# Optimization experiments

Hardware: AMD Instinct MI355X
Metric: run time of the kernel (lower is better)

The kernel has to match this reference:

```python
import jax, jax.numpy as jnp
import numpy as np

NUM_LONGTERM_MEM = 16  # config.num_longterm_mem


def setup_inputs() -> dict:
    key = jax.random.key(0)
    ks = jax.random.split(key, 9)
    B, T, C, H = 32, 2048, 768, 1536
    s = 0.02
    return {
        "x": jax.random.normal(ks[0], (B, T, C), jnp.float32),
        "Wq": jax.random.normal(ks[1], (C, C), jnp.float32) * s,
        "bq": jax.random.normal(ks[2], (C,), jnp.float32) * s,
        "W0": jax.random.normal(ks[3], (B, H, C), jnp.float32) * s,
        "b0": jax.random.normal(ks[4], (B, H), jnp.float32) * s,
        "W1": jax.random.normal(ks[5], (B, C, H), jnp.float32) * s,
        "b1": jax.random.normal(ks[6], (B, C), jnp.float32) * s,
        "Wo": jax.random.normal(ks[7], (C, C), jnp.float32) * s,
        "bo": jax.random.normal(ks[8], (C,), jnp.float32) * s,
    }


def reference(x, Wq, bq, W0, b0, W1, b1, Wo, bo):
    # x: [B, T, C]. Per-sample memory MLP weights W0 [B,H,C], W1 [B,C,H].
    B, T, C = x.shape
    L = NUM_LONGTERM_MEM
    # query projection (nn.Linear: x @ W^T + b)
    q = jnp.einsum("btc,dc->btd", x, Wq) + bq                       # [B,T,C]
    # per-sample 2-layer memory MLP with SiLU
    h = jax.nn.silu(jnp.einsum("btc,bhc->bth", q, W0) + b0[:, None, :])  # [B,T,H]
    mem = jnp.einsum("bth,bch->btc", h, W1) + b1[:, None, :]        # [B,T,C]
    # adaptive_avg_pool1d over T -> L (T divisible by L => uniform window mean)
    pooled = mem.reshape(B, L, T // L, C).mean(axis=2)              # [B,L,C]
    # output projection
    return jnp.einsum("blc,dc->bld", pooled, Wo) + bo               # [B,L,C]
```

## Files before the change

### kernel.cpp

```cpp
#include <hip/hip_runtime.h>
#include <stdint.h>

#define B_ 32
#define T_ 2048
#define C_ 768
#define H_ 1536
#define L_ 16

typedef unsigned short u16;
typedef __bf16 bf16x8 __attribute__((ext_vector_type(8)));
typedef float f32x4 __attribute__((ext_vector_type(4)));

__device__ __forceinline__ u16 f2bf(float f) {
    union { float f; uint32_t u; } v; v.f = f;
    uint32_t r = (v.u + 0x7fffu + ((v.u >> 16) & 1u)) >> 16;
    return (u16)r;
}

__device__ __forceinline__ float wave_sum(float v) {
    v += __shfl_xor(v, 1);  v += __shfl_xor(v, 2);  v += __shfl_xor(v, 4);
    v += __shfl_xor(v, 8);  v += __shfl_xor(v, 16); v += __shfl_xor(v, 32);
    return v;
}

__global__ void k_cvt(const float* __restrict__ in, u16* __restrict__ out, int n4) {
    int stride = gridDim.x * blockDim.x;
    for (int i = blockIdx.x * blockDim.x + threadIdx.x; i < n4; i += stride) {
        float4 v = reinterpret_cast<const float4*>(in)[i];
        ushort4 o;
        o.x = f2bf(v.x); o.y = f2bf(v.y); o.z = f2bf(v.z); o.w = f2bf(v.w);
        reinterpret_cast<ushort4*>(out)[i] = o;
    }
}

__global__ void k_prep1(const float* __restrict__ Wq, u16* __restrict__ WqTb,
                        const float* __restrict__ W0, u16* __restrict__ W0b,
                        const float* __restrict__ bq, const float* __restrict__ b0,
                        float* __restrict__ b0f, int e0) {
    const int t = threadIdx.x;
    if (blockIdx.x < (unsigned)e0) {
        const int w = t >> 6, lane = t & 63;
        const int nWaves = e0 * 4;
        const float4* bq4 = reinterpret_cast<const float4*>(bq);
        float4 b4_0 = bq4[lane], b4_1 = bq4[64 + lane], b4_2 = bq4[128 + lane];
        for (int rr = blockIdx.x * 4 + w; rr < B_ * H_; rr += nWaves) {
            const float4* src = reinterpret_cast<const float4*>(W0 + (size_t)rr * 768);
            ushort4* dst = reinterpret_cast<ushort4*>(W0b + (size_t)rr * 768);
            float4 v0 = src[lane], v1 = src[64 + lane], v2 = src[128 + lane];
            ushort4 o0, o1, o2;
            o0.x = f2bf(v0.x); o0.y = f2bf(v0.y); o0.z = f2bf(v0.z); o0.w = f2bf(v0.w);
            o1.x = f2bf(v1.x); o1.y = f2bf(v1.y); o1.z = f2bf(v1.z); o1.w = f2bf(v1.w);
            o2.x = f2bf(v2.x); o2.y = f2bf(v2.y); o2.z = f2bf(v2.z); o2.w = f2bf(v2.w);
            dst[lane] = o0; dst[64 + lane] = o1; dst[128 + lane] = o2;
            float dot = v0.x * b4_0.x + v0.y * b4_0.y + v0.z * b4_0.z + v0.w * b4_0.w
                      + v1.x * b4_1.x + v1.y * b4_1.y + v1.z * b4_1.z + v1.w * b4_1.w
                      + v2.x * b4_2.x + v2.y * b4_2.y + v2.z * b4_2.z + v2.w * b4_2.w;
            dot = wave_sum(dot);
            if (lane == 0) b0f[rr] = b0[rr] + dot;
        }
    } else {
        __shared__ u16 tl[64 * 65];
        const int nb = gridDim.x - e0;
        for (int tile = blockIdx.x - e0; tile < 144; tile += nb) {
            int d0 = (tile / 12) * 64, c0 = (tile % 12) * 64;
            __syncthreads();
#pragma unroll
            for (int p = 0; p < 16; ++p) {
                int idx = p * 256 + t;
                int r = idx >> 6, c = idx & 63;
                tl[r * 65 + c] = f2bf(Wq[(size_t)(d0 + r) * 768 + c0 + c]);
            }
            __syncthreads();
#pragma unroll
            for (int p = 0; p < 16; ++p) {
                int idx = p * 256 + t;
                int r = idx >> 6, c = idx & 63;
                WqTb[(size_t)(c0 + r) * 768 + d0 + c] = tl[c * 65 + r];
            }
        }
    }
}

__device__ __forceinline__ void gload16(const u16* g, u16* l) {
    __builtin_amdgcn_global_load_lds((const __attribute__((address_space(1))) void*)g,
                                     (__attribute__((address_space(3))) void*)l, 16, 0, 0);
}

template <int EPI>
__global__ __launch_bounds__(512, 2) void k_gemm9(const u16* __restrict__ Aall,
                                                  const u16* __restrict__ Ball,
                                                  const float* __restrict__ biasall,
                                                  u16* __restrict__ qout,
                                                  float* __restrict__ ph) {
    __shared__ u16 sm[81920];
    const int t = threadIdx.x;
    const int w = t >> 6, lane = t & 63;
    const int wr = w >> 2, wc = w & 3;
    const int l15 = lane & 15, kq = lane >> 4, cx = lane & 7;

    const int gx = gridDim.x, gy = gridDim.y;
    const int nwg = gx * gy * gridDim.z;
    int flat = blockIdx.x + gx * (blockIdx.y + gy * blockIdx.z);
    if ((nwg & 7) == 0) flat = (flat & 7) * (nwg >> 3) + (flat >> 3);
    const int bx = flat % gx;
    const int tmp = flat / gx;
    const int by = tmp % gy;
    const int bz = tmp / gy;

    const int n0 = bx * 256;
    const int m0 = by * 256;
    const u16* A; const u16* Bm; const float* bias;
    if constexpr (EPI == 0) {
        A = Aall + (size_t)m0 * C_;
        Bm = Ball + (size_t)n0 * C_;
        bias = biasall + n0;
    } else {
        A = Aall + ((size_t)bz * T_ + m0) * C_;
        Bm = Ball + ((size_t)bz * H_ + n0) * C_;
        bias = biasall + (size_t)bz * H_ + n0;
    }

    const int rl = (w << 4) + (lane >> 3);
    const int cs = (((lane & 7) ^ ((lane >> 3) & 7)) << 3);
    const int ldst = (w << 10);

    auto stA = [&](int kt, int buf) {
#pragma unroll
        for (int h = 0; h < 2; ++h) {
            const u16* g = A + (size_t)(h * 128 + rl) * C_ + kt * 64 + cs;
            u16* l = sm + buf * 16384 + h * 8192 + ldst;
            gload16(g, l);
            gload16(g + 8 * C_, l + 512);
        }
    };
    auto stB = [&](int kt, int buf) {
#pragma unroll
        for (int h = 0; h < 2; ++h) {
            const u16* g = Bm + (size_t)(h * 128 + rl) * C_ + kt * 64 + cs;
            u16* l = sm + 49152 + buf * 16384 + h * 8192 + ldst;
            gload16(g, l);
            gload16(g + 8 * C_, l + 512);
        }
    };

    f32x4 acc[8][4];
#pragma unroll
    for (int m = 0; m < 8; ++m)
#pragma unroll
        for (int n = 0; n < 4; ++n) acc[m][n] = (f32x4){0.f, 0.f, 0.f, 0.f};

    bf16x8 a0[4][2], a1[4][2], bfr[2][2];

    const int koff0 = ((kq ^ cx) << 3);
    const int koff1 = (((4 + kq) ^ cx) << 3);
    const u16* aB0 = sm + wr * 8192 + l15 * 64 + koff0;
    const u16* aB1 = sm + wr * 8192 + l15 * 64 + koff1;
    const u16* bB0 = sm + 49152 + (wc >> 1) * 8192 + (wc & 1) * 4096 + l15 * 64 + koff0;
    const u16* bB1 = sm + 49152 + (wc >> 1) * 8192 + (wc & 1) * 4096 + l15 * 64 + koff1;

    auto rdB0 = [&](int off) {
        bfr[0][0] = *reinterpret_cast<const bf16x8*>(bB0 + off);
        bfr[1][0] = *reinterpret_cast<const bf16x8*>(bB0 + off + 1024);
        bfr[0][1] = *reinterpret_cast<const bf16x8*>(bB1 + off);
        bfr[1][1] = *reinterpret_cast<const bf16x8*>(bB1 + off + 1024);
    };
    auto rdB1 = [&](int off) {
        bfr[0][0] = *reinterpret_cast<const bf16x8*>(bB0 + off + 2048);
        bfr[1][0] = *reinterpret_cast<const bf16x8*>(bB0 + off + 3072);
        bfr[0][1] = *reinterpret_cast<const bf16x8*>(bB1 + off + 2048);
        bfr[1][1] = *reinterpret_cast<const bf16x8*>(bB1 + off + 3072);
    };
    auto rdA0 = [&](int off) {
#pragma unroll
        for (int mm = 0; mm < 4; ++mm) {
            a0[mm][0] = *reinterpret_cast<const bf16x8*>(aB0 + off + mm * 1024);
            a0[mm][1] = *reinterpret_cast<const bf16x8*>(aB1 + off + mm * 1024);
        }
    };
    auto rdA1 = [&](int off) {
#pragma unroll
        for (int mm = 0; mm < 4; ++mm) {
            a1[mm][0] = *reinterpret_cast<const bf16x8*>(aB0 + off + 4096 + mm * 1024);
            a1[mm][1] = *reinterpret_cast<const bf16x8*>(aB1 + off + 4096 + mm * 1024);
        }
    };
    auto mma16 = [&](bf16x8 (&a)[4][2], int mq, int qn) {
        __builtin_amdgcn_s_setprio(1);
#pragma unroll
        for (int ks = 0; ks < 2; ++ks)
#pragma unroll
            for (int mm = 0; mm < 4; ++mm)
#pragma unroll
                for (int nn = 0; nn < 2; ++nn)
                    acc[mq * 4 + mm][qn * 2 + nn] = __builtin_amdgcn_mfma_f32_16x16x32_bf16(
                        a[mm][ks], bfr[nn][ks], acc[mq * 4 + mm][qn * 2 + nn], 0, 0, 0);
        __builtin_amdgcn_s_setprio(0);
    };

    stA(0, 0); stB(0, 0); stA(1, 1);
    asm volatile("s_waitcnt vmcnt(4)" ::: "memory");
    __builtin_amdgcn_s_barrier();

    int ba = 0;
#pragma unroll 1
    for (int kt = 0; kt < 12; ++kt) {
        const int bb = kt & 1;
        int ban = ba + 2; if (ban >= 3) ban -= 3;
        const bool s2 = (kt + 2 < 12);
        if (kt + 1 < 12) stB(kt + 1, bb ^ 1);
        if (s2) stA(kt + 2, ban);
        const int aoff = ba * 16384;
        const int boff = bb * 16384;
        rdB0(boff);
        rdA0(aoff);
        rdA1(aoff);
        mma16(a0, 0, 0);
        mma16(a1, 1, 0);
        __builtin_amdgcn_sched_barrier(0);
        rdB1(boff);
        mma16(a0, 0, 1);
        mma16(a1, 1, 1);
        if (s2) asm volatile("s_waitcnt vmcnt(4)" ::: "memory");
        else    asm volatile("s_waitcnt vmcnt(0)" ::: "memory");
        __builtin_amdgcn_s_barrier();
        ba = (ba + 1 == 3) ? 0 : ba + 1;
    }

    if constexpr (EPI == 0) {
        const int colb = n0 + wc * 64 + l15;
        const int rowb = m0 + wr * 128 + (kq << 2);
        float bv[4];
#pragma unroll
        for (int n = 0; n < 4; ++n) bv[n] = bias[wc * 64 + n * 16 + l15];
#pragma unroll
        for (int m = 0; m < 8; ++m)
#pragma unroll
            for (int r = 0; r < 4; ++r) {
                size_t ro = (size_t)(rowb + m * 16 + r) * C_;
#pragma unroll
                for (int n = 0; n < 4; ++n)
                    qout[ro + colb + n * 16] = f2bf(acc[m][n][r] + bv[n]);
            }
    } else {
        const int lwin = by * 2 + wr;
#pragma unroll
        for (int n = 0; n < 4; ++n) {
            int cloc = wc * 64 + n * 16 + l15;
            float bv = bias[cloc];
            float s = 0.f;
#pragma unroll
            for (int m = 0; m < 8; ++m)
#pragma unroll
                for (int r = 0; r < 4; ++r) {
                    float v = acc[m][n][r] + bv;
                    s += v / (1.f + __expf(-v));
                }
            s += __shfl_xor(s, 16);
            s += __shfl_xor(s, 32);
            if (kq == 0)
                ph[((size_t)bz * L_ + lwin) * H_ + n0 + cloc] = s * (1.f / 128.f);
        }
    }
}

__global__ __launch_bounds__(512, 2) void k_wf(const u16* __restrict__ W0b,
                                               const u16* __restrict__ WqTb,
                                               u16* __restrict__ Wfb) {
    __shared__ u16 sm[81920];
    const int t = threadIdx.x;
    const int w = t >> 6, lane = t & 63;
    const int wr = w >> 2, wc = w & 3;
    const int l15 = lane & 15, kq = lane >> 4, cx = lane & 7;

    const int gx = gridDim.x, gy = gridDim.y;
    const int nwg = gx * gy * gridDim.z;
    int flat = blockIdx.x + gx * (blockIdx.y + gy * blockIdx.z);
    if ((nwg & 7) == 0) flat = (flat & 7) * (nwg >> 3) + (flat >> 3);
    const int bx = flat % gx;
    const int tmp = flat / gx;
    const int by = tmp % gy;
    const int bz = tmp / gy;

    const int n0 = bx * 256;
    const int m0 = by * 256;
    const u16* A = W0b + ((size_t)bz * H_ + m0) * C_;
    const u16* Bm = WqTb + (size_t)n0 * C_;

    const int rl = (w << 4) + (lane >> 3);
    const int cs = (((lane & 7) ^ ((lane >> 3) & 7)) << 3);
    const int ldst = (w << 10);

    auto stA = [&](int kt, int buf) {
#pragma unroll
        for (int h = 0; h < 2; ++h) {
            const u16* g = A + (size_t)(h * 128 + rl) * C_ + kt * 64 + cs;
            u16* l = sm + buf * 16384 + h * 8192 + ldst;
            gload16(g, l);
            gload16(g + 8 * C_, l + 512);
        }
    };
    auto stB = [&](int kt, int buf) {
#pragma unroll
        for (int h = 0; h < 2; ++h) {
            const u16* g = Bm + (size_t)(h * 128 + rl) * C_ + kt * 64 + cs;
            u16* l = sm + 49152 + buf * 16384 + h * 8192 + ldst;
            gload16(g, l);
            gload16(g + 8 * C_, l + 512);
        }
    };

    f32x4 acc[8][4];
#pragma unroll
    for (int m = 0; m < 8; ++m)
#pragma unroll
        for (int n = 0; n < 4; ++n) acc[m][n] = (f32x4){0.f, 0.f, 0.f, 0.f};

    bf16x8 a0[4][2], a1[4][2], bfr[2][2];

    const int koff0 = ((kq ^ cx) << 3);
    const int koff1 = (((4 + kq) ^ cx) << 3);
    const u16* aB0 = sm + wr * 8192 + l15 * 64 + koff0;
    const u16* aB1 = sm + wr * 8192 + l15 * 64 + koff1;
    const u16* bB0 = sm + 49152 + (wc >> 1) * 8192 + (wc & 1) * 4096 + l15 * 64 + koff0;
    const u16* bB1 = sm + 49152 + (wc >> 1) * 8192 + (wc & 1) * 4096 + l15 * 64 + koff1;

    auto rdB0 = [&](int off) {
        bfr[0][0] = *reinterpret_cast<const bf16x8*>(bB0 + off);
        bfr[1][0] = *reinterpret_cast<const bf16x8*>(bB0 + off + 1024);
        bfr[0][1] = *reinterpret_cast<const bf16x8*>(bB1 + off);
        bfr[1][1] = *reinterpret_cast<const bf16x8*>(bB1 + off + 1024);
    };
    auto rdB1 = [&](int off) {
        bfr[0][0] = *reinterpret_cast<const bf16x8*>(bB0 + off + 2048);
        bfr[1][0] = *reinterpret_cast<const bf16x8*>(bB0 + off + 3072);
        bfr[0][1] = *reinterpret_cast<const bf16x8*>(bB1 + off + 2048);
        bfr[1][1] = *reinterpret_cast<const bf16x8*>(bB1 + off + 3072);
    };
    auto rdA0 = [&](int off) {
#pragma unroll
        for (int mm = 0; mm < 4; ++mm) {
            a0[mm][0] = *reinterpret_cast<const bf16x8*>(aB0 + off + mm * 1024);
            a0[mm][1] = *reinterpret_cast<const bf16x8*>(aB1 + off + mm * 1024);
        }
    };
    auto rdA1 = [&](int off) {
#pragma unroll
        for (int mm = 0; mm < 4; ++mm) {
            a1[mm][0] = *reinterpret_cast<const bf16x8*>(aB0 + off + 4096 + mm * 1024);
            a1[mm][1] = *reinterpret_cast<const bf16x8*>(aB1 + off + 4096 + mm * 1024);
        }
    };
    auto mma16 = [&](bf16x8 (&a)[4][2], int mq, int qn) {
        __builtin_amdgcn_s_setprio(1);
#pragma unroll
        for (int ks = 0; ks < 2; ++ks)
#pragma unroll
            for (int mm = 0; mm < 4; ++mm)
#pragma unroll
                for (int nn = 0; nn < 2; ++nn)
                    acc[mq * 4 + mm][qn * 2 + nn] = __builtin_amdgcn_mfma_f32_16x16x32_bf16(
                        a[mm][ks], bfr[nn][ks], acc[mq * 4 + mm][qn * 2 + nn], 0, 0, 0);
        __builtin_amdgcn_s_setprio(0);
    };

    stA(0, 0); stB(0, 0); stA(1, 1);
    asm volatile("s_waitcnt vmcnt(4)" ::: "memory");
    __builtin_amdgcn_s_barrier();

    int ba = 0;
#pragma unroll 1
    for (int kt = 0; kt < 12; ++kt) {
        const int bb = kt & 1;
        int ban = ba + 2; if (ban >= 3) ban -= 3;
        const bool s2 = (kt + 2 < 12);
        if (kt + 1 < 12) stB(kt + 1, bb ^ 1);
        if (s2) stA(kt + 2, ban);
        const int aoff = ba * 16384;
        const int boff = bb * 16384;
        rdB0(boff);
        rdA0(aoff);
        rdA1(aoff);
        mma16(a0, 0, 0);
        mma16(a1, 1, 0);
        __builtin_amdgcn_sched_barrier(0);
        rdB1(boff);
        mma16(a0, 0, 1);
        mma16(a1, 1, 1);
        if (s2) asm volatile("s_waitcnt vmcnt(4)" ::: "memory");
        else    asm volatile("s_waitcnt vmcnt(0)" ::: "memory");
        __builtin_amdgcn_s_barrier();
        ba = (ba + 1 == 3) ? 0 : ba + 1;
    }

    const int lr0 = wr * 128 + (kq << 2);
    const int lc0 = wc * 64 + l15;
#pragma unroll
    for (int m = 0; m < 8; ++m)
#pragma unroll
        for (int n = 0; n < 4; ++n)
#pragma unroll
            for (int r = 0; r < 4; ++r)
                sm[(lr0 + m * 16 + r) * 264 + lc0 + n * 16] = f2bf(acc[m][n][r]);
    __builtin_amdgcn_s_barrier();
    u16* G = Wfb + ((size_t)bz * H_ + m0) * C_ + n0;
#pragma unroll
    for (int p = 0; p < 16; ++p) {
        int fl = p * 512 + t;
        int row = fl >> 5, c8 = fl & 31;
        f32x4 v = *reinterpret_cast<const f32x4*>(&sm[row * 264 + c8 * 8]);
        *reinterpret_cast<f32x4*>(&G[(size_t)row * C_ + c8 * 8]) = v;
    }
}

__global__ __launch_bounds__(256) void k_3a(const float* __restrict__ ph,
                                            const float* __restrict__ W1,
                                            const float* __restrict__ b1,
                                            float* __restrict__ pooled) {
    const int t = threadIdx.x, w = t >> 6, lane = t & 63;
    const int b  = blockIdx.y;
    const int cb = blockIdx.x * 16 + w * 4;

    float acc[4][16];
#pragma unroll
    for (int g = 0; g < 4; ++g)
#pragma unroll
        for (int l = 0; l < 16; ++l) acc[g][l] = 0.f;

    for (int i = 0; i < H_ / 256; ++i) {
        int h0 = i * 256 + lane * 4;
        float4 wv[4];
#pragma unroll
        for (int g = 0; g < 4; ++g)
            wv[g] = *reinterpret_cast<const float4*>(W1 + ((size_t)b * C_ + cb + g) * H_ + h0);
#pragma unroll
        for (int l = 0; l < 16; ++l) {
            float4 pv = *reinterpret_cast<const float4*>(ph + ((size_t)b * L_ + l) * H_ + h0);
#pragma unroll
            for (int g = 0; g < 4; ++g)
                acc[g][l] += wv[g].x * pv.x + wv[g].y * pv.y + wv[g].z * pv.z + wv[g].w * pv.w;
        }
    }
#pragma unroll
    for (int g = 0; g < 4; ++g)
#pragma unroll
        for (int l = 0; l < 16; ++l) acc[g][l] = wave_sum(acc[g][l]);

    if (lane < 16) {
#pragma unroll
        for (int g = 0; g < 4; ++g)
            pooled[((size_t)b * L_ + lane) * C_ + cb + g] = acc[g][lane] + b1[b * C_ + cb + g];
    }
}

__global__ __launch_bounds__(256) void k_3b(const float* __restrict__ pooled,
                                            const float* __restrict__ Wo,
                                            const float* __restrict__ bo,
                                            float* __restrict__ out) {
    __shared__ __align__(16) float ps[4 * 768];
    const int t = threadIdx.x, w = t >> 6, lane = t & 63;
    const int rr0 = blockIdx.x * 4;

    for (int idx = t; idx < 4 * 768; idx += 256)
        ps[idx] = pooled[(size_t)rr0 * 768 + idx];
    __syncthreads();

    for (int d = w; d < 768; d += 4) {
        float a0 = 0.f, a1 = 0.f, a2 = 0.f, a3 = 0.f;
#pragma unroll
        for (int i = 0; i < 3; ++i) {
            int c = i * 256 + lane * 4;
            float4 wv = *reinterpret_cast<const float4*>(Wo + (size_t)d * 768 + c);
            float4 p0 = *reinterpret_cast<const float4*>(&ps[0 * 768 + c]);
            float4 p1 = *reinterpret_cast<const float4*>(&ps[1 * 768 + c]);
            float4 p2 = *reinterpret_cast<const float4*>(&ps[2 * 768 + c]);
            float4 p3 = *reinterpret_cast<const float4*>(&ps[3 * 768 + c]);
            a0 += wv.x * p0.x + wv.y * p0.y + wv.z * p0.z + wv.w * p0.w;
            a1 += wv.x * p1.x + wv.y * p1.y + wv.z * p1.z + wv.w * p1.w;
            a2 += wv.x * p2.x + wv.y * p2.y + wv.z * p2.z + wv.w * p2.w;
            a3 += wv.x * p3.x + wv.y * p3.y + wv.z * p3.z + wv.w * p3.w;
        }
        a0 = wave_sum(a0); a1 = wave_sum(a1); a2 = wave_sum(a2); a3 = wave_sum(a3);
        if (lane == 0) {
            float bb = bo[d];
            out[(size_t)(rr0 + 0) * 768 + d] = a0 + bb;
            out[(size_t)(rr0 + 1) * 768 + d] = a1 + bb;
            out[(size_t)(rr0 + 2) * 768 + d] = a2 + bb;
            out[(size_t)(rr0 + 3) * 768 + d] = a3 + bb;
        }
    }
}

extern "C" void kernel_launch(void* const* d_in, const int* in_sizes, int n_in,
                              void* d_out, int out_size, void* d_ws, size_t ws_size,
                              hipStream_t stream) {
    const float* x  = (const float*)d_in[0];
    const float* Wq = (const float*)d_in[1];
    const float* bq = (const float*)d_in[2];
    const float* W0 = (const float*)d_in[3];
    const float* b0 = (const float*)d_in[4];
    const float* W1 = (const float*)d_in[5];
    const float* b1 = (const float*)d_in[6];
    const float* Wo = (const float*)d_in[7];
    const float* bo = (const float*)d_in[8];
    float* out = (float*)d_out;

    char* p = (char*)d_ws;
    size_t off = 0;
    auto carve = [&](size_t bytes) -> char* {
        char* r = p + off;
        off += (bytes + 255) & ~(size_t)255;
        return r;
    };
    float* ph     = (float*)carve((size_t)B_ * L_ * H_ * 4);
    float* pooled = (float*)carve((size_t)B_ * L_ * C_ * 4);

    const size_t xb_bytes  = (size_t)B_ * T_ * C_ * 2;
    const size_t w0b_bytes = (size_t)B_ * H_ * C_ * 2;
    const size_t wq_bytes  = (size_t)C_ * C_ * 2;
    const size_t b0f_bytes = (size_t)B_ * H_ * 4;

    const int n4x  = B_ * T_ * C_ / 4;
    const int n4wq = C_ * C_ / 4;
    const int n4w0 = B_ * H_ * C_ / 4;

    if (off + b0f_bytes + wq_bytes + w0b_bytes + xb_bytes + 1024 <= ws_size) {
        float* b0f  = (float*)carve(b0f_bytes);
        u16*   WqTb = (u16*)carve(wq_bytes);
        u16*   Wfb  = (u16*)carve(w0b_bytes);
        u16*   U    = (u16*)carve(xb_bytes);
        u16*   W0b  = U;
        u16*   xb   = U;

        k_prep1<<<dim3(2048), 256, 0, stream>>>(Wq, WqTb, W0, W0b, bq, b0, b0f, 2016);
        k_wf<<<dim3(C_ / 256, H_ / 256, B_), 512, 0, stream>>>(W0b, WqTb, Wfb);
        k_cvt<<<dim3(2048), 256, 0, stream>>>(x, xb, n4x);
        k_gemm9<1><<<dim3(H_ / 256, T_ / 256, B_), 512, 0, stream>>>(xb, Wfb, b0f, nullptr, ph);
    } else {
        u16* qb  = (u16*)carve(xb_bytes);
        u16* Wqb = (u16*)carve(wq_bytes);
        u16* xb  = (u16*)carve(xb_bytes);
        u16* W0b = xb;
        k_cvt<<<dim3(64), 256, 0, stream>>>(Wq, Wqb, n4wq);
        k_cvt<<<dim3(2048), 256, 0, stream>>>(x, xb, n4x);
        k_gemm9<0><<<dim3(C_ / 256, (B_ * T_) / 256), 512, 0, stream>>>(xb, Wqb, bq, qb, nullptr);
        k_cvt<<<dim3(2048), 256, 0, stream>>>(W0, W0b, n4w0);
        k_gemm9<1><<<dim3(H_ / 256, T_ / 256, B_), 512, 0, stream>>>(qb, W0b, b0, nullptr, ph);
    }

    k_3a<<<dim3(C_ / 16, B_), 256, 0, stream>>>(ph, W1, b1, pooled);
    k_3b<<<dim3(B_ * L_ / 4), 256, 0, stream>>>(pooled, Wo, bo, out);
}
```

Measured before the change: 616.4 us.

## Replace pipelined 256x256 weight-fold GEMM with simple 128x128 synchronous kernel

Swaps the triple/double-buffered 256x256-tile k_wf kernel (512 threads, XOR-swizzled LDS, setprio, partial vmcnt waits) for a simpler k_wf2 using 128x128 tiles, 256 threads, and a load/sync/compute/sync loop with no software pipelining. The grid flattens batch into the M dimension, so there are more, smaller workgroups. The aim is likely better occupancy or fewer tail effects on this small per-batch GEMM. In exchange it gives up load/compute overlap, loses the LDS swizzle and so risks bank conflicts, and lowers data reuse per tile.

```diff
diff --git a/kernel.cpp b/kernel.cpp
--- a/kernel.cpp
+++ b/kernel.cpp
@@ -263,151 +263,80 @@
     }
 }
 
-__global__ __launch_bounds__(512, 2) void k_wf(const u16* __restrict__ W0b,
-                                               const u16* __restrict__ WqTb,
-                                               u16* __restrict__ Wfb) {
-    __shared__ u16 sm[81920];
-    const int t = threadIdx.x;
-    const int w = t >> 6, lane = t & 63;
-    const int wr = w >> 2, wc = w & 3;
-    const int l15 = lane & 15, kq = lane >> 4, cx = lane & 7;
-
-    const int gx = gridDim.x, gy = gridDim.y;
-    const int nwg = gx * gy * gridDim.z;
-    int flat = blockIdx.x + gx * (blockIdx.y + gy * blockIdx.z);
-    if ((nwg & 7) == 0) flat = (flat & 7) * (nwg >> 3) + (flat >> 3);
-    const int bx = flat % gx;
-    const int tmp = flat / gx;
-    const int by = tmp % gy;
-    const int bz = tmp / gy;
-
-    const int n0 = bx * 256;
-    const int m0 = by * 256;
-    const u16* A = W0b + ((size_t)bz * H_ + m0) * C_;
-    const u16* Bm = WqTb + (size_t)n0 * C_;
-
-    const int rl = (w << 4) + (lane >> 3);
-    const int cs = (((lane & 7) ^ ((lane >> 3) & 7)) << 3);
-    const int ldst = (w << 10);
-
-    auto stA = [&](int kt, int buf) {
-#pragma unroll
-        for (int h = 0; h < 2; ++h) {
-            const u16* g = A + (size_t)(h * 128 + rl) * C_ + kt * 64 + cs;
-            u16* l = sm + buf * 16384 + h * 8192 + ldst;
-            gload16(g, l);
-            gload16(g + 8 * C_, l + 512);
-        }
-    };
-    auto stB = [&](int kt, int buf) {
-#pragma unroll
-        for (int h = 0; h < 2; ++h) {
-            const u16* g = Bm + (size_t)(h * 128 + rl) * C_ + kt * 64 + cs;
-            u16* l = sm + 49152 + buf * 16384 + h * 8192 + ldst;
-            gload16(g, l);
-            gload16(g + 8 * C_, l + 512);
-        }
-    };
-
-    f32x4 acc[8][4];
-#pragma unroll
-    for (int m = 0; m < 8; ++m)
+__device__ __forceinline__ void stage_bf16_gload(const u16* gtile, int ld, u16* Ts,
+                                                 int w, int lane) {
+    const int r_in = lane >> 3;
+    const int c0   = (lane & 7) << 3;
+#pragma unroll
+    for (int j = 0; j < 4; ++j) {
+        int row = ((w << 2) + j) * 8 + r_in;
+        const u16* g = gtile + (size_t)row * ld + c0;
+        u16* l = Ts + (((w << 2) + j) << 9);
+        gload16(g, l);
+    }
+}
+
+__device__ __forceinline__ void mfma_tile(const u16* As, const u16* Bs,
+                                          f32x4 (&acc)[4][4], int wr, int wc, int lane) {
+#pragma unroll
+    for (int ks = 0; ks < 2; ++ks) {
+        const int ko = (ks << 5) + ((lane >> 4) << 3);
+        bf16x8 a[4], b[4];
+#pragma unroll
+        for (int m = 0; m < 4; ++m)
+            a[m] = *reinterpret_cast<const bf16x8*>(&As[(wr * 64 + m * 16 + (lane & 15)) * 64 + ko]);
+#pragma unroll
+        for (int n = 0; n < 4; ++n)
+            b[n] = *reinterpret_cast<const bf16x8*>(&Bs[(wc * 64 + n * 16 + (lane & 15)) * 64 + ko]);
+#pragma unroll
+        for (int m = 0; m < 4; ++m)
+#pragma unroll
+            for (int n = 0; n < 4; ++n)
+                acc[m][n] = __builtin_amdgcn_mfma_f32_16x16x32_bf16(a[m], b[n], acc[m][n], 0, 0, 0);
+    }
+}
+
+__global__ __launch_bounds__(256, 2) void k_wf2(const u16* __restrict__ W0b,
+                                                const u16* __restrict__ WqTb,
+                                                u16* __restrict__ Wfb) {
+    __shared__ u16 smw[128 * 136];
+    u16* As = smw;
+    u16* Bs = smw + 8192;
+    const int t = threadIdx.x, w = t >> 6, lane = t & 63;
+    const int wr = w >> 1, wc = w & 1;
+    const int m0 = blockIdx.y * 128;
+    const int n0 = blockIdx.x * 128;
+
+    f32x4 acc[4][4];
+#pragma unroll
+    for (int m = 0; m < 4; ++m)
 #pragma unroll
         for (int n = 0; n < 4; ++n) acc[m][n] = (f32x4){0.f, 0.f, 0.f, 0.f};
 
-    bf16x8 a0[4][2], a1[4][2], bfr[2][2];
-
-    const int koff0 = ((kq ^ cx) << 3);
-    const int koff1 = (((4 + kq) ^ cx) << 3);
-    const u16* aB0 = sm + wr * 8192 + l15 * 64 + koff0;
-    const u16* aB1 = sm + wr * 8192 + l15 * 64 + koff1;
-    const u16* bB0 = sm + 49152 + (wc >> 1) * 8192 + (wc & 1) * 4096 + l15 * 64 + koff0;
-    const u16* bB1 = sm + 49152 + (wc >> 1) * 8192 + (wc & 1) * 4096 + l15 * 64 + koff1;
-
-    auto rdB0 = [&](int off) {
-        bfr[0][0] = *reinterpret_cast<const bf16x8*>(bB0 + off);
-        bfr[1][0] = *reinterpret_cast<const bf16x8*>(bB0 + off + 1024);
-        bfr[0][1] = *reinterpret_cast<const bf16x8*>(bB1 + off);
-        bfr[1][1] = *reinterpret_cast<const bf16x8*>(bB1 + off + 1024);
-    };
-    auto rdB1 = [&](int off) {
-        bfr[0][0] = *reinterpret_cast<const bf16x8*>(bB0 + off + 2048);
-        bfr[1][0] = *reinterpret_cast<const bf16x8*>(bB0 + off + 3072);
-        bfr[0][1] = *reinterpret_cast<const bf16x8*>(bB1 + off + 2048);
-        bfr[1][1] = *reinterpret_cast<const bf16x8*>(bB1 + off + 3072);
-    };
-    auto rdA0 = [&](int off) {
-#pragma unroll
-        for (int mm = 0; mm < 4; ++mm) {
-            a0[mm][0] = *reinterpret_cast<const bf16x8*>(aB0 + off + mm * 1024);
-            a0[mm][1] = *reinterpret_cast<const bf16x8*>(aB1 + off + mm * 1024);
-        }
-    };
-    auto rdA1 = [&](int off) {
-#pragma unroll
-        for (int mm = 0; mm < 4; ++mm) {
-            a1[mm][0] = *reinterpret_cast<const bf16x8*>(aB0 + off + 4096 + mm * 1024);
-            a1[mm][1] = *reinterpret_cast<const bf16x8*>(aB1 + off + 4096 + mm * 1024);
-        }
-    };
-    auto mma16 = [&](bf16x8 (&a)[4][2], int mq, int qn) {
-        __builtin_amdgcn_s_setprio(1);
-#pragma unroll
-        for (int ks = 0; ks < 2; ++ks)
-#pragma unroll
-            for (int mm = 0; mm < 4; ++mm)
-#pragma unroll
-                for (int nn = 0; nn < 2; ++nn)
-                    acc[mq * 4 + mm][qn * 2 + nn] = __builtin_amdgcn_mfma_f32_16x16x32_bf16(
-                        a[mm][ks], bfr[nn][ks], acc[mq * 4 + mm][qn * 2 + nn], 0, 0, 0);
-        __builtin_amdgcn_s_setprio(0);
-    };
-
-    stA(0, 0); stB(0, 0); stA(1, 1);
-    asm volatile("s_waitcnt vmcnt(4)" ::: "memory");
-    __builtin_amdgcn_s_barrier();
-
-    int ba = 0;
-#pragma unroll 1
     for (int kt = 0; kt < 12; ++kt) {
-        const int bb = kt & 1;
-        int ban = ba + 2; if (ban >= 3) ban -= 3;
-        const bool s2 = (kt + 2 < 12);
-        if (kt + 1 < 12) stB(kt + 1, bb ^ 1);
-        if (s2) stA(kt + 2, ban);
-        const int aoff = ba * 16384;
-        const int boff = bb * 16384;
-        rdB0(boff);
-        rdA0(aoff);
-        rdA1(aoff);
-        mma16(a0, 0, 0);
-        mma16(a1, 1, 0);
-        __builtin_amdgcn_sched_barrier(0);
-        rdB1(boff);
-        mma16(a0, 0, 1);
-        mma16(a1, 1, 1);
-        if (s2) asm volatile("s_waitcnt vmcnt(4)" ::: "memory");
-        else    asm volatile("s_waitcnt vmcnt(0)" ::: "memory");
-        __builtin_amdgcn_s_barrier();
-        ba = (ba + 1 == 3) ? 0 : ba + 1;
-    }
-
-    const int lr0 = wr * 128 + (kq << 2);
-    const int lc0 = wc * 64 + l15;
-#pragma unroll
-    for (int m = 0; m < 8; ++m)
+        stage_bf16_gload(W0b + (size_t)m0 * C_ + kt * 64, C_, As, w, lane);
+        stage_bf16_gload(WqTb + (size_t)n0 * C_ + kt * 64, C_, Bs, w, lane);
+        __syncthreads();
+        mfma_tile(As, Bs, acc, wr, wc, lane);
+        __syncthreads();
+    }
+
+    const int lr0 = wr * 64 + ((lane >> 4) << 2);
+    const int lc0 = wc * 64 + (lane & 15);
+#pragma unroll
+    for (int m = 0; m < 4; ++m)
 #pragma unroll
         for (int n = 0; n < 4; ++n)
 #pragma unroll
             for (int r = 0; r < 4; ++r)
-                sm[(lr0 + m * 16 + r) * 264 + lc0 + n * 16] = f2bf(acc[m][n][r]);
-    __builtin_amdgcn_s_barrier();
-    u16* G = Wfb + ((size_t)bz * H_ + m0) * C_ + n0;
-#pragma unroll
-    for (int p = 0; p < 16; ++p) {
-        int fl = p * 512 + t;
-        int row = fl >> 5, c8 = fl & 31;
-        f32x4 v = *reinterpret_cast<const f32x4*>(&sm[row * 264 + c8 * 8]);
+                smw[(lr0 + m * 16 + r) * 136 + lc0 + n * 16] = f2bf(acc[m][n][r]);
+    __syncthreads();
+    u16* G = Wfb + (size_t)m0 * C_ + n0;
+#pragma unroll
+    for (int p = 0; p < 8; ++p) {
+        int fl = p * 256 + t;
+        int row = fl >> 4, c8 = fl & 15;
+        f32x4 v = *reinterpret_cast<const f32x4*>(&smw[row * 136 + c8 * 8]);
         *reinterpret_cast<f32x4*>(&G[(size_t)row * C_ + c8 * 8]) = v;
     }
 }
@@ -532,7 +461,7 @@
         u16*   xb   = U;
 
         k_prep1<<<dim3(2048), 256, 0, stream>>>(Wq, WqTb, W0, W0b, bq, b0, b0f, 2016);
-        k_wf<<<dim3(C_ / 256, H_ / 256, B_), 512, 0, stream>>>(W0b, WqTb, Wfb);
+        k_wf2<<<dim3(C_ / 128, (B_ * H_) / 128), 256, 0, stream>>>(W0b, WqTb, Wfb);
         k_cvt<<<dim3(2048), 256, 0, stream>>>(x, xb, n4x);
         k_gemm9<1><<<dim3(H_ / 256, T_ / 256, B_), 512, 0, stream>>>(xb, Wfb, b0f, nullptr, ph);
     } else {
```

New measurement: 627.3 us. Within noise of the previous version (+1.8%).
